# Optimization experiments

Hardware: AMD Instinct MI355X
Metric: run time of the kernel (lower is better)

Reference implementation:

```python
import jax, jax.numpy as jnp
import numpy as np

B, S, D, H = 4, 1500, 1280, 20
HD = D // H  # 64

def setup_inputs() -> dict:
    key = jax.random.key(0)
    ks = jax.random.split(key, 8)
    scale = 1.0 / np.sqrt(D)
    return {
        "hidden_states": jax.random.normal(ks[0], (B, S, D), dtype=jnp.float32),
        "attention_mask": jnp.zeros((B, 1, S, S), dtype=jnp.float32),
        "q_w": jax.random.normal(ks[1], (D, D), dtype=jnp.float32) * scale,
        "q_b": jax.random.normal(ks[2], (D,), dtype=jnp.float32) * 0.02,
        "k_w": jax.random.normal(ks[3], (D, D), dtype=jnp.float32) * scale,
        "v_w": jax.random.normal(ks[4], (D, D), dtype=jnp.float32) * scale,
        "v_b": jax.random.normal(ks[5], (D,), dtype=jnp.float32) * 0.02,
        "o_w": jax.random.normal(ks[6], (D, D), dtype=jnp.float32) * scale,
        "o_b": jax.random.normal(ks[7], (D,), dtype=jnp.float32) * 0.02,
    }

def reference(hidden_states, attention_mask, q_w, q_b, k_w, v_w, v_b, o_w, o_b):
    bsz, seq_len, d_model = hidden_states.shape
    scaling = HD ** (-0.5)
    # Projections (k_proj has NO bias, matching the module)
    q = hidden_states @ q_w + q_b
    k = hidden_states @ k_w
    v = hidden_states @ v_w + v_b
    # [B, H, S, HD]
    q = q.reshape(bsz, seq_len, H, HD).transpose(0, 2, 1, 3)
    k = k.reshape(bsz, seq_len, H, HD).transpose(0, 2, 1, 3)
    v = v.reshape(bsz, seq_len, H, HD).transpose(0, 2, 1, 3)
    scores = jnp.einsum("bhqd,bhkd->bhqk", q, k) * scaling
    scores = scores + attention_mask
    attn = jax.nn.softmax(scores.astype(jnp.float32), axis=-1).astype(q.dtype)
    out = jnp.einsum("bhqk,bhkd->bhqd", attn, v)
    out = out.transpose(0, 2, 1, 3).reshape(bsz, seq_len, d_model)
    return out @ o_w + o_b
```

## Files before the change

kernel.cpp:

```cpp
#include <hip/hip_runtime.h>
#include <hip/hip_bf16.h>
#include <cstddef>

#define B_   4
#define S_   1500
#define D_   1280
#define H_   20
#define HD_  64
#define M_   (B_*S_)
#define SPAD 1536
#define BIGNEG (-1e30f)
#define LOG2E 1.44269504088896340736f
#define KVB  64
#define NTA  24

typedef short bf16x8 __attribute__((ext_vector_type(8)));
typedef float f32x4 __attribute__((ext_vector_type(4)));
typedef unsigned short u16;
typedef u16 u16x8 __attribute__((ext_vector_type(8)));
typedef unsigned int u32x4v __attribute__((ext_vector_type(4)));

#define MFMA __builtin_amdgcn_mfma_f32_16x16x32_bf16

__device__ __forceinline__ u16 f2bf(float f) {
  union { float f; unsigned u; } x; x.f = f;
  unsigned r = (x.u + 0x7fffu + ((x.u >> 16) & 1u)) >> 16;
  return (u16)r;
}

__device__ __forceinline__ unsigned cvtpk(float a, float b) {
  unsigned r;
  asm volatile("v_cvt_pk_bf16_f32 %0, %1, %2" : "=v"(r) : "v"(a), "v"(b));
  return r;
}

__device__ __forceinline__ void gl_lds16(const u16* g, u16* l) {
  typedef __attribute__((address_space(1))) const unsigned GU;
  typedef __attribute__((address_space(3))) unsigned LU;
  __builtin_amdgcn_global_load_lds((GU*)g, (LU*)l, 16, 0, 0);
}

__global__ __launch_bounds__(256) void k_conv(const float* __restrict__ X, u16* __restrict__ Y) {
  size_t i = (size_t)blockIdx.x * 256 + threadIdx.x;
  const float4* p = (const float4*)(X + i * 8);
  float4 a = p[0], b = p[1];
  u16x8 v;
  v[0]=f2bf(a.x); v[1]=f2bf(a.y); v[2]=f2bf(a.z); v[3]=f2bf(a.w);
  v[4]=f2bf(b.x); v[5]=f2bf(b.y); v[6]=f2bf(b.z); v[7]=f2bf(b.w);
  *(u16x8*)(Y + i * 8) = v;
}

__global__ __launch_bounds__(256) void k_mscan(const float* __restrict__ m, int* __restrict__ flag) {
  const size_t tot = (size_t)B_ * S_ * S_;
  size_t i = ((size_t)blockIdx.x * 256 + threadIdx.x) * 4;
  size_t stride = (size_t)gridDim.x * 256 * 4;
  for (; i < tot; i += stride) {
    float4 v = *(const float4*)(m + i);
    if (v.x != 0.f || v.y != 0.f || v.z != 0.f || v.w != 0.f) {
      int b = (int)(i / ((size_t)S_ * S_));
      atomicOr(&flag[b], 1);
    }
  }
}

__global__ __launch_bounds__(256) void k_trans4(const float* __restrict__ qw,
                                                const float* __restrict__ kw,
                                                const float* __restrict__ vw,
                                                const float* __restrict__ ow,
                                                u16* __restrict__ Wt) {
  const float* W = (blockIdx.z == 0) ? qw : (blockIdx.z == 1) ? kw
                   : (blockIdx.z == 2) ? vw : ow;
  u16* dst = Wt + (size_t)blockIdx.z * D_ * D_;
  __shared__ float t[32][33];
  int n0 = blockIdx.x * 32, k0 = blockIdx.y * 32;
  int tx = threadIdx.x & 31, ty = threadIdx.x >> 5;
  #pragma unroll
  for (int i = ty; i < 32; i += 8) t[i][tx] = W[(size_t)(k0 + i) * D_ + n0 + tx];
  __syncthreads();
  #pragma unroll
  for (int i = ty; i < 32; i += 8) dst[(size_t)(n0 + i) * D_ + k0 + tx] = f2bf(t[tx][i]);
}

__global__ __launch_bounds__(256) void k_vtrans(const u16* __restrict__ Vb, u16* __restrict__ Vt) {
  __shared__ u16 t[128][72];
  int bh = blockIdx.x, b = bh / H_, h = bh % H_;
  int s0 = blockIdx.y * 128;
  int tid = threadIdx.x;
  #pragma unroll
  for (int r = 0; r < 4; r++) {
    int sl = r * 32 + (tid >> 3);
    int s = s0 + sl; if (s > S_ - 1) s = S_ - 1;
    bf16x8 v = *(const bf16x8*)(Vb + ((size_t)(b * S_ + s)) * D_ + h * HD_ + (tid & 7) * 8);
    *(bf16x8*)&t[sl][(tid & 7) * 8] = v;
  }
  __syncthreads();
  #pragma unroll
  for (int r = 0; r < 4; r++) {
    int d = r * 16 + (tid >> 4);
    int ss = (tid & 15) * 8;
    u16x8 o;
    #pragma unroll
    for (int q = 0; q < 8; q++) {
      int sl = ss + q;
      int kk = ((sl >> 4) & 3) * 4 + (sl & 3) + ((sl >> 2) & 3) * 16 + (sl & 64);
      o[q] = t[kk][d];
    }
    *(u16x8*)(Vt + ((size_t)bh * HD_ + d) * SPAD + s0 + ss) = o;
  }
}

__global__ __launch_bounds__(256) void k_gemmqkv(const u16* __restrict__ A,
                                                 const u16* __restrict__ Wt,
                                                 const float* __restrict__ q_b,
                                                 const float* __restrict__ v_b,
                                                 u16* __restrict__ Qb) {
  int p = blockIdx.x;
  int gg = p & 7;
  int idx = p >> 3;
  int y = idx / 6;
  int x = gg * 6 + idx % 6;
  if (x >= 47) return;

  __shared__ u16 As[2][128 * 64];
  __shared__ u16 Bs[2][128 * 64];
  int tid = threadIdx.x;
  int lane = tid & 63;
  int wv = tid >> 6;
  int l16 = lane & 15, lg = lane >> 4;
  int wr = wv >> 1, wc = wv & 1;
  int m0 = x * 128;
  int n0g = y * 128;
  int sel = y / 10;
  int nloc = n0g - sel * 1280;

  int srow = tid >> 3;
  int csw = ((tid & 7) ^ (srow & 7)) * 8;
  const u16* asrc = A + csw;
  const u16* bsrc = Wt + csw;
  int dbase = wv * 8 * 64;

  f32x4 acc[4][4] = {};

#define STAGEG(tt, bufb) do {                                            \
    int kk0 = (tt) * 64;                                                 \
    _Pragma("unroll")                                                    \
    for (int c = 0; c < 4; c++) {                                        \
      int row = srow + c * 32;                                           \
      int ar = m0 + row; if (ar > M_ - 1) ar = M_ - 1;                   \
      gl_lds16(asrc + (size_t)ar * D_ + kk0,                             \
               &As[bufb][0] + dbase + c * 2048);                         \
      gl_lds16(bsrc + (size_t)(n0g + row) * D_ + kk0,                    \
               &Bs[bufb][0] + dbase + c * 2048);                         \
    }                                                                    \
  } while (0)

  STAGEG(0, 0);
  __syncthreads();
  for (int t = 0; t < 20; t++) {
    int cb = t & 1;
    if (t < 19) STAGEG(t + 1, cb ^ 1);
    const u16* AsC = &As[cb][0];
    const u16* BsC = &Bs[cb][0];
    #pragma unroll
    for (int kk = 0; kk < 2; kk++) {
      int pcol = ((kk * 4 + lg) ^ (l16 & 7)) * 8;
      bf16x8 af[4], bf[4];
      #pragma unroll
      for (int m = 0; m < 4; m++)
        af[m] = *(const bf16x8*)&AsC[(wr * 64 + m * 16 + l16) * 64 + pcol];
      #pragma unroll
      for (int n = 0; n < 4; n++)
        bf[n] = *(const bf16x8*)&BsC[(wc * 64 + n * 16 + l16) * 64 + pcol];
      __builtin_amdgcn_s_setprio(1);
      #pragma unroll
      for (int m = 0; m < 4; m++)
        #pragma unroll
        for (int n = 0; n < 4; n++)
          acc[m][n] = MFMA(af[m], bf[n], acc[m][n], 0, 0, 0);
      __builtin_amdgcn_s_setprio(0);
    }
    __syncthreads();
  }
#undef STAGEG

  const float* bias = (sel == 0) ? q_b : v_b;
  float scl = (sel == 0) ? (0.125f * LOG2E) : 1.0f;
  u16* outb = Qb + (size_t)sel * ((size_t)M_ * D_);

  #pragma unroll
  for (int m = 0; m < 4; m++) {
    int row0 = m0 + wr * 64 + m * 16 + lg * 4;
    #pragma unroll
    for (int n = 0; n < 4; n++) {
      int colL = nloc + wc * 64 + n * 16 + l16;
      float bv = (sel == 1) ? 0.0f : bias[colL];
      #pragma unroll
      for (int j = 0; j < 4; j++) {
        int row = row0 + j;
        if (row < M_) {
          float v = (acc[m][n][j] + bv) * scl;
          outb[(size_t)row * D_ + colL] = f2bf(v);
        }
      }
    }
  }
}

__global__ __launch_bounds__(256) void k_gemmo(const u16* __restrict__ A,
                                               const u16* __restrict__ Wt,
                                               const float* __restrict__ bias,
                                               float* __restrict__ outp) {
  int p = blockIdx.x;
  int gg = p & 7;
  int idx = p >> 3;
  int y = idx / 6;
  int x = gg * 6 + idx % 6;
  if (x >= 47) return;

  __shared__ u16 As[2][128 * 64];
  __shared__ u16 Bs[2][128 * 64];
  int tid = threadIdx.x;
  int lane = tid & 63;
  int wv = tid >> 6;
  int l16 = lane & 15, lg = lane >> 4;
  int wr = wv >> 1, wc = wv & 1;
  int m0 = x * 128, n0 = y * 128;

  int srow = tid >> 3;
  int csw = ((tid & 7) ^ (srow & 7)) * 8;
  const u16* asrc = A + csw;
  const u16* bsrc = Wt + csw;
  int dbase = wv * 8 * 64;

  f32x4 acc[4][4] = {};

#define STAGEG(tt, bufb) do {                                            \
    int kk0 = (tt) * 64;                                                 \
    _Pragma("unroll")                                                    \
    for (int c = 0; c < 4; c++) {                                        \
      int row = srow + c * 32;                                           \
      int ar = m0 + row; if (ar > M_ - 1) ar = M_ - 1;                   \
      gl_lds16(asrc + (size_t)ar * D_ + kk0,                             \
               &As[bufb][0] + dbase + c * 2048);                         \
      gl_lds16(bsrc + (size_t)(n0 + row) * D_ + kk0,                     \
               &Bs[bufb][0] + dbase + c * 2048);                         \
    }                                                                    \
  } while (0)

  STAGEG(0, 0);
  __syncthreads();
  for (int t = 0; t < 20; t++) {
    int cb = t & 1;
    if (t < 19) STAGEG(t + 1, cb ^ 1);
    const u16* AsC = &As[cb][0];
    const u16* BsC = &Bs[cb][0];
    #pragma unroll
    for (int kk = 0; kk < 2; kk++) {
      int pcol = ((kk * 4 + lg) ^ (l16 & 7)) * 8;
      bf16x8 af[4], bf[4];
      #pragma unroll
      for (int m = 0; m < 4; m++)
        af[m] = *(const bf16x8*)&AsC[(wr * 64 + m * 16 + l16) * 64 + pcol];
      #pragma unroll
      for (int n = 0; n < 4; n++)
        bf[n] = *(const bf16x8*)&BsC[(wc * 64 + n * 16 + l16) * 64 + pcol];
      __builtin_amdgcn_s_setprio(1);
      #pragma unroll
      for (int m = 0; m < 4; m++)
        #pragma unroll
        for (int n = 0; n < 4; n++)
          acc[m][n] = MFMA(af[m], bf[n], acc[m][n], 0, 0, 0);
      __builtin_amdgcn_s_setprio(0);
    }
    __syncthreads();
  }
#undef STAGEG

  #pragma unroll
  for (int m = 0; m < 4; m++) {
    int row0 = m0 + wr * 64 + m * 16 + lg * 4;
    #pragma unroll
    for (int n = 0; n < 4; n++) {
      int col = n0 + wc * 64 + n * 16 + l16;
      float bv = bias[col];
      #pragma unroll
      for (int j = 0; j < 4; j++) {
        int row = row0 + j;
        if (row < M_) outp[(size_t)row * D_ + col] = acc[m][n][j] + bv;
      }
    }
  }
}

__global__ __launch_bounds__(256) void k_attn(const u16* __restrict__ Qb,
                                              const u16* __restrict__ Kb,
                                              const u16* __restrict__ Vt,
                                              const float* __restrict__ mask,
                                              const int* __restrict__ mflag,
                                              u16* __restrict__ Ctx) {
  __shared__ u16 Kl[2][64 * 64];
  __shared__ u16 Vl[2][64 * 64];

  int p = blockIdx.x;
  int L = (p & 7) * 120 + (p >> 3);
  int h = L % 20;
  int g = L / 20;
  int b = g / 12;
  int xq = g % 12;
  int bh = b * H_ + h;
  int um = mflag[b];

  int tid = threadIdx.x;
  int lane = tid & 63, wv = tid >> 6;
  int l16 = lane & 15, lg = lane >> 4;
  int qw0 = xq * 128 + wv * 16;

  int qr0 = qw0 + l16;      if (qr0 > S_ - 1) qr0 = S_ - 1;
  int qr1 = qw0 + 64 + l16; if (qr1 > S_ - 1) qr1 = S_ - 1;
  const u16* qp0 = Qb + ((size_t)(b * S_ + qr0)) * D_ + h * HD_ + lg * 8;
  const u16* qp1 = Qb + ((size_t)(b * S_ + qr1)) * D_ + h * HD_ + lg * 8;
  bf16x8 aq00 = *(const bf16x8*)(qp0);
  bf16x8 aq01 = *(const bf16x8*)(qp0 + 32);
  bf16x8 aq10 = *(const bf16x8*)(qp1);
  bf16x8 aq11 = *(const bf16x8*)(qp1 + 32);
  const float* mrow0 = mask + (size_t)b * S_ * S_ + (size_t)qr0 * S_;
  const float* mrow1 = mask + (size_t)b * S_ * S_ + (size_t)qr1 * S_;

  int sr0 = wv * 16 + (lane >> 3);
  int csw = ((lane & 7) ^ (lane >> 3)) * 8;
  const u16* ksrc = Kb + (size_t)b * S_ * D_ + h * HD_ + csw;
  const u16* vsrc0 = Vt + ((size_t)bh * HD_ + sr0) * SPAD + csw;
  const u16* vsrc1 = vsrc0 + 8 * SPAD;

  float m0_ = BIGNEG, l0_ = 0.0f, m1_ = BIGNEG, l1_ = 0.0f;
  f32x4 acc0[4] = {}, acc1[4] = {};
  const f32x4 zf = {0, 0, 0, 0};

#define STAGE(k0s, bufb) do {                                          \
    int key0_ = (k0s) + sr0;     if (key0_ > S_ - 1) key0_ = S_ - 1;   \
    int key1_ = key0_ + 8;       if (key1_ > S_ - 1) key1_ = S_ - 1;   \
    u16* kd_ = &Kl[bufb][0] + wv * 1024;                               \
    u16* vd_ = &Vl[bufb][0] + wv * 1024;                               \
    gl_lds16(ksrc + (size_t)key0_ * D_, kd_);                          \
    gl_lds16(ksrc + (size_t)key1_ * D_, kd_ + 512);                    \
    gl_lds16(vsrc0 + (k0s), vd_);                                      \
    gl_lds16(vsrc1 + (k0s), vd_ + 512);                                \
  } while (0)

#define SMX(sv, mm, ll, accv) do {                                     \
    float t0 = fmaxf(fmaxf(sv[0][0], sv[0][1]), fmaxf(sv[0][2], sv[0][3])); \
    float t1 = fmaxf(fmaxf(sv[1][0], sv[1][1]), fmaxf(sv[1][2], sv[1][3])); \
    float t2 = fmaxf(fmaxf(sv[2][0], sv[2][1]), fmaxf(sv[2][2], sv[2][3])); \
    float t3 = fmaxf(fmaxf(sv[3][0], sv[3][1]), fmaxf(sv[3][2], sv[3][3])); \
    float rmax = fmaxf(fmaxf(t0, t1), fmaxf(t2, t3));                  \
    rmax = fmaxf(rmax, __shfl_xor(rmax, 16));                          \
    rmax = fmaxf(rmax, __shfl_xor(rmax, 32));                          \
    float mn = fmaxf(mm, rmax);                                        \
    if (!__all(mn - mm <= 8.0f)) {                                     \
      float c = __builtin_amdgcn_exp2f(mm - mn);                       \
      mm = mn; ll *= c;                                                \
      _Pragma("unroll")                                                \
      for (int j = 0; j < 4; j++) {                                    \
        float cj = __shfl(c, lg * 4 + j);                              \
        accv[0][j] *= cj; accv[1][j] *= cj;                            \
        accv[2][j] *= cj; accv[3][j] *= cj;                            \
      }                                                                \
    }                                                                  \
    _Pragma("unroll")                                                  \
    for (int sub = 0; sub < 4; sub++)                                  \
      _Pragma("unroll")                                                \
      for (int j = 0; j < 4; j++)                                      \
        sv[sub][j] = __builtin_amdgcn_exp2f(sv[sub][j] - mm);          \
    float a0 = (sv[0][0] + sv[0][1]) + (sv[0][2] + sv[0][3]);          \
    float a1 = (sv[1][0] + sv[1][1]) + (sv[1][2] + sv[1][3]);          \
    float a2 = (sv[2][0] + sv[2][1]) + (sv[2][2] + sv[2][3]);          \
    float a3 = (sv[3][0] + sv[3][1]) + (sv[3][2] + sv[3][3]);          \
    ll += (a0 + a1) + (a2 + a3);                                       \
  } while (0)

#define COMPUTE(curb, k0_, LASTV) do {                                 \
    const u16* KlC = &Kl[curb][0];                                     \
    const u16* VlC = &Vl[curb][0];                                     \
    f32x4 s0[4], s1[4];                                                \
    __builtin_amdgcn_s_setprio(1);                                     \
    _Pragma("unroll")                                                  \
    for (int sub = 0; sub < 4; sub++) {                                \
      const u16* kb = KlC + (sub * 16 + l16) * 64;                     \
      bf16x8 kf0 = *(const bf16x8*)(kb + ((lg     ^ (l16 & 7)) * 8));  \
      bf16x8 kf1 = *(const bf16x8*)(kb + (((4+lg) ^ (l16 & 7)) * 8));  \
      s0[sub] = MFMA(kf0, aq00, zf, 0, 0, 0);                          \
      s0[sub] = MFMA(kf1, aq01, s0[sub], 0, 0, 0);                     \
      s1[sub] = MFMA(kf0, aq10, zf, 0, 0, 0);                          \
      s1[sub] = MFMA(kf1, aq11, s1[sub], 0, 0, 0);                     \
    }                                                                  \
    __builtin_amdgcn_s_setprio(0);                                     \
    if (um) {   \
      _Pragma("unroll")                                                \
      for (int sub = 0; sub < 4; sub++) {                              \
        int mc = (k0_) + sub * 16 + lg * 4;                            \
        if (mc > S_ - 4) mc = S_ - 4;                                  \
        float4 mv0 = *(const float4*)(mrow0 + mc);                     \
        float4 mv1 = *(const float4*)(mrow1 + mc);                     \
        s0[sub][0] = fmaf(mv0.x, LOG2E, s0[sub][0]);                   \
        s0[sub][1] = fmaf(mv0.y, LOG2E, s0[sub][1]);                   \
        s0[sub][2] = fmaf(mv0.z, LOG2E, s0[sub][2]);                   \
        s0[sub][3] = fmaf(mv0.w, LOG2E, s0[sub][3]);                   \
        s1[sub][0] = fmaf(mv1.x, LOG2E, s1[sub][0]);                   \
        s1[sub][1] = fmaf(mv1.y, LOG2E, s1[sub][1]);                   \
        s1[sub][2] = fmaf(mv1.z, LOG2E, s1[sub][2]);                   \
        s1[sub][3] = fmaf(mv1.w, LOG2E, s1[sub][3]);                   \
      }                                                                \
    }                                                                  \
    if (LASTV) {                                                       \
      _Pragma("unroll")                                                \
      for (int sub = 0; sub < 4; sub++) {                              \
        int kb_ = (k0_) + sub * 16 + lg * 4;                           \
        _Pragma("unroll")                                              \
        for (int j = 0; j < 4; j++)                                    \
          if (kb_ + j >= S_) { s0[sub][j] = BIGNEG; s1[sub][j] = BIGNEG; } \
      }                                                                \
    }                                                                  \
    SMX(s0, m0_, l0_, acc0);                                           \
    union { u32x4v u; bf16x8 bf; } pA0, pA1;                           \
    pA0.u[0] = cvtpk(s0[0][0], s0[0][1]); pA0.u[1] = cvtpk(s0[0][2], s0[0][3]); \
    pA0.u[2] = cvtpk(s0[1][0], s0[1][1]); pA0.u[3] = cvtpk(s0[1][2], s0[1][3]); \
    pA1.u[0] = cvtpk(s0[2][0], s0[2][1]); pA1.u[1] = cvtpk(s0[2][2], s0[2][3]); \
    pA1.u[2] = cvtpk(s0[3][0], s0[3][1]); pA1.u[3] = cvtpk(s0[3][2], s0[3][3]); \
    SMX(s1, m1_, l1_, acc1);                                           \
    union { u32x4v u; bf16x8 bf; } pB0, pB1;                           \
    pB0.u[0] = cvtpk(s1[0][0], s1[0][1]); pB0.u[1] = cvtpk(s1[0][2], s1[0][3]); \
    pB0.u[2] = cvtpk(s1[1][0], s1[1][1]); pB0.u[3] = cvtpk(s1[1][2], s1[1][3]); \
    pB1.u[0] = cvtpk(s1[2][0], s1[2][1]); pB1.u[1] = cvtpk(s1[2][2], s1[2][3]); \
    pB1.u[2] = cvtpk(s1[3][0], s1[3][1]); pB1.u[3] = cvtpk(s1[3][2], s1[3][3]); \
    __builtin_amdgcn_s_setprio(1);                                     \
    _Pragma("unroll")                                                  \
    for (int n = 0; n < 4; n++) {                                      \
      const u16* vb = VlC + (n * 16 + l16) * 64;                       \
      bf16x8 bv0 = *(const bf16x8*)(vb + (((lg*2  ) ^ (l16 & 7)) * 8));\
      bf16x8 bv1 = *(const bf16x8*)(vb + (((lg*2+1) ^ (l16 & 7)) * 8));\
      acc0[n] = MFMA(pA0.bf, bv0, acc0[n], 0, 0, 0);                   \
      acc0[n] = MFMA(pA1.bf, bv1, acc0[n], 0, 0, 0);                   \
      acc1[n] = MFMA(pB0.bf, bv0, acc1[n], 0, 0, 0);                   \
      acc1[n] = MFMA(pB1.bf, bv1, acc1[n], 0, 0, 0);                   \
    }                                                                  \
    __builtin_amdgcn_s_setprio(0);                                     \
  } while (0)

  STAGE(0, 0);

  for (int t = 0; t < NTA - 1; t++) {
    int k0 = t * KVB;
    __builtin_amdgcn_s_barrier();
    asm volatile("" ::: "memory");
    STAGE(k0 + KVB, (t + 1) & 1);
    asm volatile("s_waitcnt vmcnt(4)" ::: "memory");
    __builtin_amdgcn_s_barrier();
    asm volatile("" ::: "memory");
    COMPUTE(t & 1, k0, false);
  }
  {
    const int k0 = (NTA - 1) * KVB;
    __builtin_amdgcn_s_barrier();
    asm volatile("s_waitcnt vmcnt(0)" ::: "memory");
    __builtin_amdgcn_s_barrier();
    asm volatile("" ::: "memory");
    COMPUTE((NTA - 1) & 1, k0, true);
  }

  l0_ += __shfl_xor(l0_, 16);
  l0_ += __shfl_xor(l0_, 32);
  l1_ += __shfl_xor(l1_, 16);
  l1_ += __shfl_xor(l1_, 32);
  float inv0 = 1.0f / l0_;
  float inv1 = 1.0f / l1_;
  #pragma unroll
  for (int j = 0; j < 4; j++) {
    float ivj0 = __shfl(inv0, lg * 4 + j);
    float ivj1 = __shfl(inv1, lg * 4 + j);
    int row0 = qw0 + lg * 4 + j;
    int row1 = row0 + 64;
    if (row0 < S_) {
      #pragma unroll
      for (int n = 0; n < 4; n++)
        Ctx[((size_t)(b * S_ + row0)) * D_ + h * HD_ + n * 16 + l16] = f2bf(acc0[n][j] * ivj0);
    }
    if (row1 < S_) {
      #pragma unroll
      for (int n = 0; n < 4; n++)
        Ctx[((size_t)(b * S_ + row1)) * D_ + h * HD_ + n * 16 + l16] = f2bf(acc1[n][j] * ivj1);
    }
  }
#undef STAGE
#undef SMX
#undef COMPUTE
}

extern "C" void kernel_launch(void* const* d_in, const int* in_sizes, int n_in,
                              void* d_out, int out_size, void* d_ws, size_t ws_size,
                              hipStream_t stream) {
  const float* hs   = (const float*)d_in[0];
  const float* mask = (const float*)d_in[1];
  const float* q_w  = (const float*)d_in[2];
  const float* q_b  = (const float*)d_in[3];
  const float* k_w  = (const float*)d_in[4];
  const float* v_w  = (const float*)d_in[5];
  const float* v_b  = (const float*)d_in[6];
  const float* o_w  = (const float*)d_in[7];
  const float* o_b  = (const float*)d_in[8];
  float* out = (float*)d_out;

  char* w = (char*)d_ws;
  const size_t XD = (size_t)M_ * D_;
  const size_t WD = (size_t)D_ * D_;
  u16* Xb  = (u16*)(w);                 w += XD * 2;
  u16* Wtq = (u16*)(w);                 w += WD * 2;
  u16* Wtk = (u16*)(w);                 w += WD * 2;
  u16* Wtv = (u16*)(w);                 w += WD * 2;
  u16* Wto = (u16*)(w);                 w += WD * 2;
  u16* Qb  = (u16*)(w);                 w += XD * 2;
  u16* Kb  = (u16*)(w);                 w += XD * 2;
  u16* Vb  = (u16*)(w);                 w += XD * 2;
  u16* Vt  = (u16*)(w);                 w += (size_t)B_ * H_ * HD_ * SPAD * 2;
  int* mflag = (int*)(w);               w += 4 * sizeof(int);
  u16* Ctx = Xb;
  (void)Wtk; (void)Wtv;

  hipMemsetAsync(mflag, 0, 4 * sizeof(int), stream);
  k_mscan<<<dim3(2048), dim3(256), 0, stream>>>(mask, mflag);

  k_conv<<<dim3(3750), dim3(256), 0, stream>>>(hs, Xb);
  k_trans4<<<dim3(40, 40, 4), dim3(256), 0, stream>>>(q_w, k_w, v_w, o_w, Wtq);

  k_gemmqkv<<<dim3(1440), dim3(256), 0, stream>>>(Xb, Wtq, q_b, v_b, Qb);
  k_vtrans<<<dim3(80, 12), dim3(256), 0, stream>>>(Vb, Vt);

  k_attn<<<dim3(960), dim3(256), 0, stream>>>(Qb, Kb, Vt, mask, mflag, Ctx);

  k_gemmo<<<dim3(480), dim3(256), 0, stream>>>(Ctx, Wto, o_b, out);
}
```

Before: 244.4 us.

## Replace double-buffered LDS staging with single buffer in projection GEMMs

Both the QKV and output projection GEMMs drop the double-buffered shared-memory tiles and use one buffer. Each k-step now loads its tile, synchronises, then computes, so the global-to-LDS prefetch no longer overlaps the MFMA work. This halves LDS use per block, which may let more blocks share a CU, at the cost of exposed load latency. The loop also ends each step with the existing barrier, so the next load waits for all waves to finish reading.

```diff
diff --git a/kernel.cpp b/kernel.cpp
--- a/kernel.cpp
+++ b/kernel.cpp
@@ -121,8 +121,8 @@
   int x = gg * 6 + idx % 6;
   if (x >= 47) return;
 
-  __shared__ u16 As[2][128 * 64];
-  __shared__ u16 Bs[2][128 * 64];
+  __shared__ u16 As[128 * 64];
+  __shared__ u16 Bs[128 * 64];
   int tid = threadIdx.x;
   int lane = tid & 63;
   int wv = tid >> 6;
@@ -141,36 +141,31 @@
 
   f32x4 acc[4][4] = {};
 
-#define STAGEG(tt, bufb) do {                                            \
+#define STAGEG(tt) do {                                                  \
     int kk0 = (tt) * 64;                                                 \
     _Pragma("unroll")                                                    \
     for (int c = 0; c < 4; c++) {                                        \
       int row = srow + c * 32;                                           \
       int ar = m0 + row; if (ar > M_ - 1) ar = M_ - 1;                   \
-      gl_lds16(asrc + (size_t)ar * D_ + kk0,                             \
-               &As[bufb][0] + dbase + c * 2048);                         \
+      gl_lds16(asrc + (size_t)ar * D_ + kk0, &As[0] + dbase + c * 2048); \
       gl_lds16(bsrc + (size_t)(n0g + row) * D_ + kk0,                    \
-               &Bs[bufb][0] + dbase + c * 2048);                         \
+               &Bs[0] + dbase + c * 2048);                               \
     }                                                                    \
   } while (0)
 
-  STAGEG(0, 0);
-  __syncthreads();
   for (int t = 0; t < 20; t++) {
-    int cb = t & 1;
-    if (t < 19) STAGEG(t + 1, cb ^ 1);
-    const u16* AsC = &As[cb][0];
-    const u16* BsC = &Bs[cb][0];
+    STAGEG(t);
+    __syncthreads();
     #pragma unroll
     for (int kk = 0; kk < 2; kk++) {
       int pcol = ((kk * 4 + lg) ^ (l16 & 7)) * 8;
       bf16x8 af[4], bf[4];
       #pragma unroll
       for (int m = 0; m < 4; m++)
-        af[m] = *(const bf16x8*)&AsC[(wr * 64 + m * 16 + l16) * 64 + pcol];
+        af[m] = *(const bf16x8*)&As[(wr * 64 + m * 16 + l16) * 64 + pcol];
       #pragma unroll
       for (int n = 0; n < 4; n++)
-        bf[n] = *(const bf16x8*)&BsC[(wc * 64 + n * 16 + l16) * 64 + pcol];
+        bf[n] = *(const bf16x8*)&Bs[(wc * 64 + n * 16 + l16) * 64 + pcol];
       __builtin_amdgcn_s_setprio(1);
       #pragma unroll
       for (int m = 0; m < 4; m++)
@@ -217,8 +212,8 @@
   int x = gg * 6 + idx % 6;
   if (x >= 47) return;
 
-  __shared__ u16 As[2][128 * 64];
-  __shared__ u16 Bs[2][128 * 64];
+  __shared__ u16 As[128 * 64];
+  __shared__ u16 Bs[128 * 64];
   int tid = threadIdx.x;
   int lane = tid & 63;
   int wv = tid >> 6;
@@ -234,36 +229,31 @@
 
   f32x4 acc[4][4] = {};
 
-#define STAGEG(tt, bufb) do {                                            \
+#define STAGEG(tt) do {                                                  \
     int kk0 = (tt) * 64;                                                 \
     _Pragma("unroll")                                                    \
     for (int c = 0; c < 4; c++) {                                        \
       int row = srow + c * 32;                                           \
       int ar = m0 + row; if (ar > M_ - 1) ar = M_ - 1;                   \
-      gl_lds16(asrc + (size_t)ar * D_ + kk0,                             \
-               &As[bufb][0] + dbase + c * 2048);                         \
+      gl_lds16(asrc + (size_t)ar * D_ + kk0, &As[0] + dbase + c * 2048); \
       gl_lds16(bsrc + (size_t)(n0 + row) * D_ + kk0,                     \
-               &Bs[bufb][0] + dbase + c * 2048);                         \
+               &Bs[0] + dbase + c * 2048);                               \
     }                                                                    \
   } while (0)
 
-  STAGEG(0, 0);
-  __syncthreads();
   for (int t = 0; t < 20; t++) {
-    int cb = t & 1;
-    if (t < 19) STAGEG(t + 1, cb ^ 1);
-    const u16* AsC = &As[cb][0];
-    const u16* BsC = &Bs[cb][0];
+    STAGEG(t);
+    __syncthreads();
     #pragma unroll
     for (int kk = 0; kk < 2; kk++) {
       int pcol = ((kk * 4 + lg) ^ (l16 & 7)) * 8;
       bf16x8 af[4], bf[4];
       #pragma unroll
       for (int m = 0; m < 4; m++)
-        af[m] = *(const bf16x8*)&AsC[(wr * 64 + m * 16 + l16) * 64 + pcol];
+        af[m] = *(const bf16x8*)&As[(wr * 64 + m * 16 + l16) * 64 + pcol];
       #pragma unroll
       for (int n = 0; n < 4; n++)
-        bf[n] = *(const bf16x8*)&BsC[(wc * 64 + n * 16 + l16) * 64 + pcol];
+        bf[n] = *(const bf16x8*)&Bs[(wc * 64 + n * 16 + l16) * 64 + pcol];
       __builtin_amdgcn_s_setprio(1);
       #pragma unroll
       for (int m = 0; m < 4; m++)
@@ -394,7 +384,7 @@
       s1[sub] = MFMA(kf1, aq11, s1[sub], 0, 0, 0);                     \
     }                                                                  \
     __builtin_amdgcn_s_setprio(0);                                     \
-    if (um) {   \
+    if (um) {                                                          \
       _Pragma("unroll")                                                \
       for (int sub = 0; sub < 4; sub++) {                              \
         int mc = (k0_) + sub * 16 + lg * 4;                            \
```

Measured after the change: 226.7 us. 7.2% less time.
